# Optimization experiments

Hardware: AMD Instinct MI355X
Metric: run time of the kernel (lower is better)

Reference implementation:

```python
import jax, jax.numpy as jnp
import numpy as np

B, S, E = 8, 2048, 512
VOCAB, FVOCAB = 32000, 128
SCALE = float(np.power(E, 0.5))  # emb_size ** (0.5 * temper), temper=1


def setup_inputs() -> dict:
    key = jax.random.key(0)
    ks = jax.random.split(key, 7)
    key_seq = jax.random.randint(ks[0], (B, S), 0, VOCAB, dtype=jnp.int32)
    value_seq = jax.random.randint(ks[1], (B, S), 0, FVOCAB, dtype=jnp.int32)
    hidden = jax.random.normal(ks[2], (B, S, E), dtype=jnp.float32)
    mask_matrix = jax.random.uniform(ks[3], (B, S, S), dtype=jnp.float32)
    nan_matrix = jnp.zeros((1,), dtype=jnp.int32)  # unused by forward
    # learned params; padding_idx=0 -> zero row in embeddings
    key_emb = jax.random.normal(ks[4], (VOCAB, E), dtype=jnp.float32).at[0].set(0.0)
    value_emb = jax.random.normal(ks[5], (FVOCAB, E), dtype=jnp.float32).at[0].set(0.0)
    weight = jax.random.normal(ks[6], (E, E), dtype=jnp.float32) / np.sqrt(E)
    return {
        "key_seq": key_seq, "value_seq": value_seq, "hidden": hidden,
        "mask_matrix": mask_matrix, "nan_matrix": nan_matrix,
        "key_emb": key_emb, "value_emb": value_emb, "weight": weight,
    }


def reference(key_seq, value_seq, hidden, mask_matrix, nan_matrix,
              key_emb, value_emb, weight):
    k = key_emb[key_seq]          # [B,S,E]
    v = value_emb[value_seq]      # [B,S,E]
    q = jnp.einsum('bsd,de->bse', hidden, weight)   # hidden @ weight
    u = jnp.einsum('bse,bte->bst', q, k) / SCALE    # QK^T, [B,S,S]
    mask = jnp.clip(mask_matrix.astype(u.dtype), 0.0, 1.0)
    exp_u = jnp.exp(u)
    delta = exp_u * mask
    p = delta / (jnp.sum(delta, axis=2, keepdims=True) + 1e-10)
    o = jnp.einsum('bst,bte->bse', p, v)            # PV, [B,S,E]
    return o
```

## Files before the change

kernel.cpp:

```cpp
#include <hip/hip_runtime.h>
#include <stdint.h>

#define BB 8
#define SS 2048
#define EE 512
#define INV_SCALE 0.04419417382415922f

typedef __attribute__((ext_vector_type(8))) short bf8_t;
typedef __attribute__((ext_vector_type(4))) float f4_t;

__device__ __forceinline__ unsigned short f2bf(float f) {
    union { float f; uint32_t u; } x; x.f = f;
    uint32_t r = x.u + 0x7fffu + ((x.u >> 16) & 1u);
    return (unsigned short)(r >> 16);
}


__global__ void __launch_bounds__(256) gather_k_kernel(const int* __restrict__ idx,
                                                       const float* __restrict__ emb,
                                                       unsigned short* __restrict__ out) {
    int id = blockIdx.x * 256 + threadIdx.x;
    int chunk = id & 63;
    int row = id >> 6;
    int e0 = chunk * 8;
    int k = idx[row];
    const float* src = emb + (size_t)k * EE + e0;
    float4 a = *(const float4*)(src);
    float4 c = *(const float4*)(src + 4);
    union { unsigned short s[8]; int4 v; } u;
    u.s[0] = f2bf(a.x); u.s[1] = f2bf(a.y); u.s[2] = f2bf(a.z); u.s[3] = f2bf(a.w);
    u.s[4] = f2bf(c.x); u.s[5] = f2bf(c.y); u.s[6] = f2bf(c.z); u.s[7] = f2bf(c.w);
    *(int4*)(out + (size_t)row * EE + e0) = u.v;
}

__global__ void __launch_bounds__(256) cast_h_kernel(const float* __restrict__ in,
                                                     unsigned short* __restrict__ out) {
    int id = blockIdx.x * 256 + threadIdx.x;
    const float* src = in + (size_t)id * 8;
    float4 a = *(const float4*)(src);
    float4 c = *(const float4*)(src + 4);
    union { unsigned short s[8]; int4 v; } u;
    u.s[0] = f2bf(a.x); u.s[1] = f2bf(a.y); u.s[2] = f2bf(a.z); u.s[3] = f2bf(a.w);
    u.s[4] = f2bf(c.x); u.s[5] = f2bf(c.y); u.s[6] = f2bf(c.z); u.s[7] = f2bf(c.w);
    *(int4*)(out + (size_t)id * 8) = u.v;
}

__global__ void __launch_bounds__(256) gather_vt_kernel(const int* __restrict__ idx,
                                                        const float* __restrict__ emb,
                                                        unsigned short* __restrict__ vt) {
    int id = blockIdx.x * 256 + threadIdx.x;
    int t = id & (SS - 1);
    int rest = id >> 11;
    int e = rest & (EE - 1);
    int b = rest >> 9;
    int k = idx[b * SS + t];
    vt[id] = f2bf(emb[(size_t)k * EE + e]);
}

__global__ void __launch_bounds__(256) transpose_w_kernel(const float* __restrict__ w,
                                                          unsigned short* __restrict__ wt) {
    int id = blockIdx.x * 256 + threadIdx.x;
    int e = id & (EE - 1);
    int f = id >> 9;
    wt[id] = f2bf(w[(size_t)e * EE + f] * INV_SCALE);
}


__device__ __forceinline__ void stage_tile(const unsigned short* gbase, int ld, int k0,
                                           unsigned short* lds, int wave, int lane) {
    const int srcchunk = ((lane & 3) ^ ((lane >> 3) & 3)) * 8;
#pragma unroll
    for (int i = 0; i < 2; ++i) {
        int row = i * 64 + wave * 16 + (lane >> 2);
        const unsigned short* g = gbase + (size_t)row * ld + (k0 + srcchunk);
        unsigned short* l = lds + i * 2048 + wave * 512 + lane * 8;
        __builtin_amdgcn_global_load_lds((const __attribute__((address_space(1))) unsigned int*)g,
                                         (__attribute__((address_space(3))) unsigned int*)l,
                                         16, 0, 0);
    }
}

template <int KLEN>
__device__ __forceinline__ void mfma_loop(const unsigned short* Abase, int lda,
                                          const unsigned short* Bbase, int ldb,
                                          unsigned short* As, unsigned short* Bs,
                                          f4_t acc[4][4], int wave, int lane) {
    const int wm = wave >> 1, wn = wave & 1, quad = lane >> 4, l16 = lane & 15;
    const int qs = (quad ^ ((l16 >> 1) & 3)) * 8;
    constexpr int NT = KLEN / 32;

    stage_tile(Abase, lda, 0, As, wave, lane);
    stage_tile(Bbase, ldb, 0, Bs, wave, lane);
    __syncthreads();

    int cur = 0;
#pragma unroll 1
    for (int t = 0; t < NT; ++t) {
        if (t + 1 < NT) {
            stage_tile(Abase, lda, (t + 1) * 32, As + ((cur ^ 1) << 12), wave, lane);
            stage_tile(Bbase, ldb, (t + 1) * 32, Bs + ((cur ^ 1) << 12), wave, lane);
        }
        const unsigned short* a = As + (cur << 12);
        const unsigned short* b = Bs + (cur << 12);
        bf8_t af[4], bfr[4];
#pragma unroll
        for (int mi = 0; mi < 4; ++mi)
            af[mi] = *(const bf8_t*)(a + (wm * 64 + mi * 16 + l16) * 32 + qs);
#pragma unroll
        for (int ni = 0; ni < 4; ++ni)
            bfr[ni] = *(const bf8_t*)(b + (wn * 64 + ni * 16 + l16) * 32 + qs);
#pragma unroll
        for (int mi = 0; mi < 4; ++mi)
#pragma unroll
            for (int ni = 0; ni < 4; ++ni)
                acc[mi][ni] = __builtin_amdgcn_mfma_f32_16x16x32_bf16(af[mi], bfr[ni],
                                                                      acc[mi][ni], 0, 0, 0);
        __syncthreads();
        cur ^= 1;
    }
}

__global__ void __launch_bounds__(256) qgen_kernel(const unsigned short* __restrict__ H,
                                                   const unsigned short* __restrict__ Wt,
                                                   unsigned short* __restrict__ Q) {
    __shared__ unsigned short As[2 * 128 * 32];
    __shared__ unsigned short Bs[2 * 128 * 32];
    const int tid = threadIdx.x, wave = tid >> 6, lane = tid & 63;
    const int rowT = blockIdx.y;
    const int colT = blockIdx.x;
    f4_t acc[4][4];
    const f4_t z = {0.f, 0.f, 0.f, 0.f};
    for (int i = 0; i < 4; ++i) for (int j = 0; j < 4; ++j) acc[i][j] = z;
    mfma_loop<EE>(H + (size_t)rowT * 128 * EE, EE,
                  Wt + (size_t)colT * 128 * EE, EE, As, Bs, acc, wave, lane);
    const int wm = wave >> 1, wn = wave & 1, quad = lane >> 4, l16 = lane & 15;
#pragma unroll
    for (int mi = 0; mi < 4; ++mi)
#pragma unroll
        for (int r = 0; r < 4; ++r) {
            int row = rowT * 128 + wm * 64 + mi * 16 + quad * 4 + r;
#pragma unroll
            for (int ni = 0; ni < 4; ++ni) {
                int col = colT * 128 + wn * 64 + ni * 16 + l16;
                Q[(size_t)row * EE + col] = f2bf(acc[mi][ni][r]);
            }
        }
}

__global__ void __launch_bounds__(256) pv_kernel(const unsigned short* __restrict__ delta,
                                                 const unsigned short* __restrict__ Vt,
                                                 const float* __restrict__ lsum,
                                                 float* __restrict__ out) {
    __shared__ unsigned short As[2 * 128 * 32];
    __shared__ unsigned short Bs[2 * 128 * 32];
    const int tid = threadIdx.x, wave = tid >> 6, lane = tid & 63;
    const int b = blockIdx.z, qT = blockIdx.y, eT = blockIdx.x;
    f4_t acc[4][4];
    const f4_t z = {0.f, 0.f, 0.f, 0.f};
    for (int i = 0; i < 4; ++i) for (int j = 0; j < 4; ++j) acc[i][j] = z;
    mfma_loop<SS>(delta + ((size_t)b * SS + qT * 128) * SS, SS,
                  Vt + ((size_t)b * EE + eT * 128) * SS, SS, As, Bs, acc, wave, lane);
    const int wm = wave >> 1, wn = wave & 1, quad = lane >> 4, l16 = lane & 15;
#pragma unroll
    for (int mi = 0; mi < 4; ++mi)
#pragma unroll
        for (int r = 0; r < 4; ++r) {
            int row = qT * 128 + wm * 64 + mi * 16 + quad * 4 + r;
            float inv = 1.0f / (lsum[b * SS + row] + 1e-10f);
#pragma unroll
            for (int ni = 0; ni < 4; ++ni) {
                int col = eT * 128 + wn * 64 + ni * 16 + l16;
                out[((size_t)b * SS + row) * EE + col] = acc[mi][ni][r] * inv;
            }
        }
}


__device__ __forceinline__ void stage_half(const unsigned short* base, int t, int kh,
                                           unsigned short* half_, int tid) {
#pragma unroll
    for (int j = 0; j < 2; ++j) {
        int idx = j * 512 + tid;
        int r = idx >> 2, slot = idx & 3;
        int c4 = slot ^ ((r >> 1) & 3);
        const unsigned short* g = base + (size_t)r * EE + t * 64 + kh * 32 + c4 * 8;
        __builtin_amdgcn_global_load_lds((const __attribute__((address_space(1))) unsigned int*)g,
                                         (__attribute__((address_space(3))) unsigned int*)(half_ + idx * 8),
                                         16, 0, 0);
    }
}

template <int NH, int WAIT>
__device__ __forceinline__ void qk8_phase(const unsigned short* Ah, const unsigned short* Bh,
                                          bf8_t af[8], f4_t acc[8][4],
                                          const unsigned short* sbase, int st, int skh,
                                          unsigned short* sdst, bool sen,
                                          int wm, int wn, int l16, int aslot, int tid,
                                          bool lastsel) {
    if (NH == 0) {
#pragma unroll
        for (int mi = 0; mi < 8; ++mi)
            af[mi] = *(const bf8_t*)(Ah + (wm * 128 + mi * 16 + l16) * 32 + aslot);
    }
    bf8_t b0 = *(const bf8_t*)(Bh + (wn * 64 + NH * 32 + l16) * 32 + aslot);
    bf8_t b1 = *(const bf8_t*)(Bh + (wn * 64 + NH * 32 + 16 + l16) * 32 + aslot);
    if (sen) stage_half(sbase, st, skh, sdst, tid);
    if (WAIT >= 0) {
        if (lastsel) asm volatile("s_waitcnt vmcnt(0)" ::: "memory");
        else         asm volatile("s_waitcnt vmcnt(6)" ::: "memory");
    }
    __builtin_amdgcn_s_barrier();
    asm volatile("s_waitcnt lgkmcnt(0)" ::: "memory");
    __builtin_amdgcn_sched_barrier(0);
    __builtin_amdgcn_s_setprio(1);
#pragma unroll
    for (int mi = 0; mi < 8; ++mi) {
        acc[mi][NH * 2]     = __builtin_amdgcn_mfma_f32_16x16x32_bf16(af[mi], b0, acc[mi][NH * 2], 0, 0, 0);
        acc[mi][NH * 2 + 1] = __builtin_amdgcn_mfma_f32_16x16x32_bf16(af[mi], b1, acc[mi][NH * 2 + 1], 0, 0, 0);
    }
    __builtin_amdgcn_s_setprio(0);
    __builtin_amdgcn_s_barrier();
    __builtin_amdgcn_sched_barrier(0);
}

__global__ void __launch_bounds__(512, 2) qk8_kernel(const unsigned short* __restrict__ Q,
                                                     const unsigned short* __restrict__ K,
                                                     const float* __restrict__ mask,
                                                     unsigned short* __restrict__ delta,
                                                     float* __restrict__ lsum) {
    __shared__ unsigned short Ab[2][2][256 * 32];
    __shared__ unsigned short Bb[2][2][256 * 32];
    const int tid = threadIdx.x;
    const int wave = tid >> 6, lane = tid & 63;
    const int wm = wave >> 2, wn = wave & 3;
    const int quad = lane >> 4, l16 = lane & 15;
    const int aslot = (quad ^ ((l16 >> 1) & 3)) * 8;

    const int lin = blockIdx.x;
    const int b = lin & 7;
    const int rest = lin >> 3;
    const int tT = rest & 7, qT = rest >> 3;

    const unsigned short* Abase = Q + ((size_t)b * SS + qT * 256) * EE;
    const unsigned short* Bbase = K + ((size_t)b * SS + tT * 256) * EE;

    f4_t acc[8][4];
    const f4_t z = {0.f, 0.f, 0.f, 0.f};
#pragma unroll
    for (int i = 0; i < 8; ++i)
#pragma unroll
        for (int j = 0; j < 4; ++j) acc[i][j] = z;

    stage_half(Abase, 0, 0, &Ab[0][0][0], tid);
    stage_half(Bbase, 0, 0, &Bb[0][0][0], tid);
    stage_half(Abase, 0, 1, &Ab[0][1][0], tid);
    stage_half(Bbase, 0, 1, &Bb[0][1][0], tid);
    stage_half(Abase, 1, 0, &Ab[1][0][0], tid);
    stage_half(Bbase, 1, 0, &Bb[1][0][0], tid);
    stage_half(Abase, 1, 1, &Ab[1][1][0], tid);
    asm volatile("s_waitcnt vmcnt(6)" ::: "memory");
    __builtin_amdgcn_s_barrier();
    __builtin_amdgcn_sched_barrier(0);

    bf8_t af[8];

#pragma unroll 1
    for (int it = 0; it < 4; ++it) {
        const int t1 = 2 * it + 1, t2 = 2 * it + 2, t3 = 2 * it + 3;
        const bool last = (it == 3);
        qk8_phase<0, -1>(&Ab[0][0][0], &Bb[0][0][0], af, acc, Bbase, t1, 1, &Bb[1][1][0], true,  wm, wn, l16, aslot, tid, last);
        qk8_phase<1, -1>(&Ab[0][0][0], &Bb[0][0][0], af, acc, Abase, t2, 0, &Ab[0][0][0], !last, wm, wn, l16, aslot, tid, last);
        qk8_phase<0, -1>(&Ab[0][1][0], &Bb[0][1][0], af, acc, Bbase, t2, 0, &Bb[0][0][0], !last, wm, wn, l16, aslot, tid, last);
        qk8_phase<1,  6>(&Ab[0][1][0], &Bb[0][1][0], af, acc, Abase, t2, 1, &Ab[0][1][0], !last, wm, wn, l16, aslot, tid, last);
        qk8_phase<0, -1>(&Ab[1][0][0], &Bb[1][0][0], af, acc, Bbase, t2, 1, &Bb[0][1][0], !last, wm, wn, l16, aslot, tid, last);
        qk8_phase<1, -1>(&Ab[1][0][0], &Bb[1][0][0], af, acc, Abase, t3, 0, &Ab[1][0][0], !last, wm, wn, l16, aslot, tid, last);
        qk8_phase<0, -1>(&Ab[1][1][0], &Bb[1][1][0], af, acc, Bbase, t3, 0, &Bb[1][0][0], !last, wm, wn, l16, aslot, tid, last);
        qk8_phase<1,  6>(&Ab[1][1][0], &Bb[1][1][0], af, acc, Abase, t3, 1, &Ab[1][1][0], !last, wm, wn, l16, aslot, tid, last);
    }

#pragma unroll
    for (int mi = 0; mi < 8; ++mi) {
#pragma unroll
        for (int r = 0; r < 4; ++r) {
            int row = qT * 256 + wm * 128 + mi * 16 + quad * 4 + r;
            const float* mrow = mask + ((size_t)b * SS + row) * SS;
            unsigned short* drow = delta + ((size_t)b * SS + row) * SS;
            float psum = 0.f;
#pragma unroll
            for (int j = 0; j < 4; ++j) {
                int col = tT * 256 + wn * 64 + j * 16 + l16;
                float m = mrow[col];
                m = fminf(fmaxf(m, 0.f), 1.f);
                float e = __expf(acc[mi][j][r]) * m;
                drow[col] = f2bf(e);
                psum += e;
            }
#pragma unroll
            for (int off = 1; off < 16; off <<= 1)
                psum += __shfl_xor(psum, off, 16);
            if (l16 == 0) atomicAdd(&lsum[b * SS + row], psum);
        }
    }
}


extern "C" void kernel_launch(void* const* d_in, const int* in_sizes, int n_in,
                              void* d_out, int out_size, void* d_ws, size_t ws_size,
                              hipStream_t stream) {
    const int*   key_seq = (const int*)d_in[0];
    const int*   val_seq = (const int*)d_in[1];
    const float* hidden  = (const float*)d_in[2];
    const float* mask    = (const float*)d_in[3];
    const float* key_emb = (const float*)d_in[5];
    const float* val_emb = (const float*)d_in[6];
    const float* weight  = (const float*)d_in[7];
    float* out = (float*)d_out;

    char* ws = (char*)d_ws;
    const size_t SZ_BSE = (size_t)BB * SS * EE * sizeof(unsigned short);
    unsigned short* Q    = (unsigned short*)(ws);
    unsigned short* K    = (unsigned short*)(ws + SZ_BSE);
    unsigned short* Vt   = (unsigned short*)(ws + 2 * SZ_BSE);
    unsigned short* H    = (unsigned short*)(ws + 3 * SZ_BSE);
    unsigned short* Wt   = (unsigned short*)(ws + 4 * SZ_BSE);
    float*          lsum = (float*)(ws + 4 * SZ_BSE + 524288);
    unsigned short* delta= (unsigned short*)(ws + 4 * SZ_BSE + 524288 + 65536);

    hipMemsetAsync(lsum, 0, (size_t)BB * SS * sizeof(float), stream);

    gather_k_kernel<<<4096, 256, 0, stream>>>(key_seq, key_emb, K);
    cast_h_kernel<<<4096, 256, 0, stream>>>(hidden, H);
    gather_vt_kernel<<<32768, 256, 0, stream>>>(val_seq, val_emb, Vt);
    transpose_w_kernel<<<1024, 256, 0, stream>>>(weight, Wt);

    qgen_kernel<<<dim3(4, 128), 256, 0, stream>>>(H, Wt, Q);
    qk8_kernel<<<512, 512, 0, stream>>>(Q, K, mask, delta, lsum);
    pv_kernel<<<dim3(4, 16, 8), 256, 0, stream>>>(delta, Vt, lsum, out);
}
```

Measured before the change: 428.2 us.

## Replace PV GEMM with 256x128-tile, 8-wave pipelined kernel using direct-to-LDS loads

The old 128x128 PV kernel built on the generic mfma loop is replaced by a 512-thread kernel that computes 256x128 output tiles. It stages A/B halves into LDS with global_load_lds in a multi-buffered pipeline, using explicit vmcnt waits, barriers and setprio around the MFMA phases, and uses batch-interleaved block ordering. The V-transpose gather also writes 8 bf16 values per thread as one 16-byte store instead of one value per thread. This targets global-memory traffic and latency in the largest GEMM, at the cost of more registers and LDS per block and fragile hand-tuned wait counts.

```diff
diff --git a/kernel.cpp b/kernel.cpp
--- a/kernel.cpp
+++ b/kernel.cpp
@@ -49,12 +49,19 @@
                                                         const float* __restrict__ emb,
                                                         unsigned short* __restrict__ vt) {
     int id = blockIdx.x * 256 + threadIdx.x;
-    int t = id & (SS - 1);
-    int rest = id >> 11;
+    int t8 = id & 255;
+    int rest = id >> 8;
     int e = rest & (EE - 1);
     int b = rest >> 9;
-    int k = idx[b * SS + t];
-    vt[id] = f2bf(emb[(size_t)k * EE + e]);
+    int t0 = t8 * 8;
+    const int* ib = idx + b * SS + t0;
+    union { unsigned short s[8]; int4 v; } u;
+#pragma unroll
+    for (int j = 0; j < 8; ++j) {
+        int k = ib[j];
+        u.s[j] = f2bf(emb[(size_t)k * EE + e]);
+    }
+    *(int4*)(vt + ((size_t)b * EE + e) * SS + t0) = u.v;
 }
 
 __global__ void __launch_bounds__(256) transpose_w_kernel(const float* __restrict__ w,
@@ -147,34 +154,6 @@
         }
 }
 
-__global__ void __launch_bounds__(256) pv_kernel(const unsigned short* __restrict__ delta,
-                                                 const unsigned short* __restrict__ Vt,
-                                                 const float* __restrict__ lsum,
-                                                 float* __restrict__ out) {
-    __shared__ unsigned short As[2 * 128 * 32];
-    __shared__ unsigned short Bs[2 * 128 * 32];
-    const int tid = threadIdx.x, wave = tid >> 6, lane = tid & 63;
-    const int b = blockIdx.z, qT = blockIdx.y, eT = blockIdx.x;
-    f4_t acc[4][4];
-    const f4_t z = {0.f, 0.f, 0.f, 0.f};
-    for (int i = 0; i < 4; ++i) for (int j = 0; j < 4; ++j) acc[i][j] = z;
-    mfma_loop<SS>(delta + ((size_t)b * SS + qT * 128) * SS, SS,
-                  Vt + ((size_t)b * EE + eT * 128) * SS, SS, As, Bs, acc, wave, lane);
-    const int wm = wave >> 1, wn = wave & 1, quad = lane >> 4, l16 = lane & 15;
-#pragma unroll
-    for (int mi = 0; mi < 4; ++mi)
-#pragma unroll
-        for (int r = 0; r < 4; ++r) {
-            int row = qT * 128 + wm * 64 + mi * 16 + quad * 4 + r;
-            float inv = 1.0f / (lsum[b * SS + row] + 1e-10f);
-#pragma unroll
-            for (int ni = 0; ni < 4; ++ni) {
-                int col = eT * 128 + wn * 64 + ni * 16 + l16;
-                out[((size_t)b * SS + row) * EE + col] = acc[mi][ni][r] * inv;
-            }
-        }
-}
-
 
 __device__ __forceinline__ void stage_half(const unsigned short* base, int t, int kh,
                                            unsigned short* half_, int tid) {
@@ -304,6 +283,124 @@
 }
 
 
+__device__ __forceinline__ void stage_halfA(const unsigned short* base, int t, int kh,
+                                            unsigned short* half_, int tid) {
+#pragma unroll
+    for (int j = 0; j < 2; ++j) {
+        int idx = j * 512 + tid;
+        int r = idx >> 2, slot = idx & 3;
+        int c4 = slot ^ ((r >> 1) & 3);
+        const unsigned short* g = base + (size_t)r * SS + t * 64 + kh * 32 + c4 * 8;
+        __builtin_amdgcn_global_load_lds((const __attribute__((address_space(1))) unsigned int*)g,
+                                         (__attribute__((address_space(3))) unsigned int*)(half_ + idx * 8),
+                                         16, 0, 0);
+    }
+}
+
+__device__ __forceinline__ void stage_halfB(const unsigned short* base, int t, int kh,
+                                            unsigned short* half_, int tid) {
+    int r = tid >> 2, slot = tid & 3;
+    int c4 = slot ^ ((r >> 1) & 3);
+    const unsigned short* g = base + (size_t)r * SS + t * 64 + kh * 32 + c4 * 8;
+    __builtin_amdgcn_global_load_lds((const __attribute__((address_space(1))) unsigned int*)g,
+                                     (__attribute__((address_space(3))) unsigned int*)(half_ + tid * 8),
+                                     16, 0, 0);
+}
+
+template <int VM>
+__device__ __forceinline__ void pv8_phase(const unsigned short* Ah, const unsigned short* Bh,
+                                          f4_t acc[8][2],
+                                          const unsigned short* Abase, const unsigned short* Bbase,
+                                          int st, int skh, unsigned short* dA, unsigned short* dB,
+                                          bool sen,
+                                          int wm, int wn, int l16, int aslot, int tid) {
+    bf8_t af[8];
+#pragma unroll
+    for (int mi = 0; mi < 8; ++mi)
+        af[mi] = *(const bf8_t*)(Ah + (wm * 128 + mi * 16 + l16) * 32 + aslot);
+    bf8_t b0 = *(const bf8_t*)(Bh + (wn * 32 + l16) * 32 + aslot);
+    bf8_t b1 = *(const bf8_t*)(Bh + (wn * 32 + 16 + l16) * 32 + aslot);
+    if (sen) { stage_halfA(Abase, st, skh, dA, tid); stage_halfB(Bbase, st, skh, dB, tid); }
+    if (VM == 6)      asm volatile("s_waitcnt vmcnt(6)" ::: "memory");
+    else if (VM == 3) asm volatile("s_waitcnt vmcnt(3)" ::: "memory");
+    else              asm volatile("s_waitcnt vmcnt(0)" ::: "memory");
+    __builtin_amdgcn_s_barrier();
+    asm volatile("s_waitcnt lgkmcnt(0)" ::: "memory");
+    __builtin_amdgcn_sched_barrier(0);
+    __builtin_amdgcn_s_setprio(1);
+#pragma unroll
+    for (int mi = 0; mi < 8; ++mi) {
+        acc[mi][0] = __builtin_amdgcn_mfma_f32_16x16x32_bf16(af[mi], b0, acc[mi][0], 0, 0, 0);
+        acc[mi][1] = __builtin_amdgcn_mfma_f32_16x16x32_bf16(af[mi], b1, acc[mi][1], 0, 0, 0);
+    }
+    __builtin_amdgcn_s_setprio(0);
+    __builtin_amdgcn_s_barrier();
+    __builtin_amdgcn_sched_barrier(0);
+}
+
+__global__ void __launch_bounds__(512, 2) pv8_kernel(const unsigned short* __restrict__ delta,
+                                                     const unsigned short* __restrict__ Vt,
+                                                     const float* __restrict__ lsum,
+                                                     float* __restrict__ out) {
+    __shared__ unsigned short Ab[2][2][256 * 32];
+    __shared__ unsigned short Bb[2][2][128 * 32];
+    const int tid = threadIdx.x;
+    const int wave = tid >> 6, lane = tid & 63;
+    const int wm = wave >> 2, wn = wave & 3;
+    const int quad = lane >> 4, l16 = lane & 15;
+    const int aslot = (quad ^ ((l16 >> 1) & 3)) * 8;
+
+    const int lin = blockIdx.x;
+    const int b = lin & 7;
+    const int qT = (lin >> 3) & 7;
+    const int eT = lin >> 6;
+
+    const unsigned short* Abase = delta + ((size_t)b * SS + qT * 256) * SS;
+    const unsigned short* Bbase = Vt + ((size_t)b * EE + eT * 128) * SS;
+
+    f4_t acc[8][2];
+    const f4_t z = {0.f, 0.f, 0.f, 0.f};
+#pragma unroll
+    for (int i = 0; i < 8; ++i) { acc[i][0] = z; acc[i][1] = z; }
+
+    stage_halfA(Abase, 0, 0, &Ab[0][0][0], tid); stage_halfB(Bbase, 0, 0, &Bb[0][0][0], tid);
+    stage_halfA(Abase, 0, 1, &Ab[0][1][0], tid); stage_halfB(Bbase, 0, 1, &Bb[0][1][0], tid);
+    stage_halfA(Abase, 1, 0, &Ab[1][0][0], tid); stage_halfB(Bbase, 1, 0, &Bb[1][0][0], tid);
+    asm volatile("s_waitcnt vmcnt(6)" ::: "memory");
+    __builtin_amdgcn_s_barrier();
+    __builtin_amdgcn_sched_barrier(0);
+
+#pragma unroll 1
+    for (int it = 0; it < 16; ++it) {
+        const int t1 = 2 * it + 1, t2 = 2 * it + 2, t3 = 2 * it + 3;
+        if (it < 15) {
+            pv8_phase<6>(&Ab[0][0][0], &Bb[0][0][0], acc, Abase, Bbase, t1, 1, &Ab[1][1][0], &Bb[1][1][0], true, wm, wn, l16, aslot, tid);
+            pv8_phase<6>(&Ab[0][1][0], &Bb[0][1][0], acc, Abase, Bbase, t2, 0, &Ab[0][0][0], &Bb[0][0][0], true, wm, wn, l16, aslot, tid);
+            pv8_phase<6>(&Ab[1][0][0], &Bb[1][0][0], acc, Abase, Bbase, t2, 1, &Ab[0][1][0], &Bb[0][1][0], true, wm, wn, l16, aslot, tid);
+            pv8_phase<6>(&Ab[1][1][0], &Bb[1][1][0], acc, Abase, Bbase, t3, 0, &Ab[1][0][0], &Bb[1][0][0], true, wm, wn, l16, aslot, tid);
+        } else {
+            pv8_phase<6>(&Ab[0][0][0], &Bb[0][0][0], acc, Abase, Bbase, t1, 1, &Ab[1][1][0], &Bb[1][1][0], true, wm, wn, l16, aslot, tid);
+            pv8_phase<6>(&Ab[0][1][0], &Bb[0][1][0], acc, Abase, Bbase, 0, 0, (unsigned short*)0, (unsigned short*)0, false, wm, wn, l16, aslot, tid);
+            pv8_phase<3>(&Ab[1][0][0], &Bb[1][0][0], acc, Abase, Bbase, 0, 0, (unsigned short*)0, (unsigned short*)0, false, wm, wn, l16, aslot, tid);
+            pv8_phase<0>(&Ab[1][1][0], &Bb[1][1][0], acc, Abase, Bbase, 0, 0, (unsigned short*)0, (unsigned short*)0, false, wm, wn, l16, aslot, tid);
+        }
+    }
+
+#pragma unroll
+    for (int mi = 0; mi < 8; ++mi) {
+#pragma unroll
+        for (int r = 0; r < 4; ++r) {
+            const int row = qT * 256 + wm * 128 + mi * 16 + quad * 4 + r;
+            const float inv = 1.0f / (lsum[b * SS + row] + 1e-10f);
+            const size_t orow = ((size_t)b * SS + row) * EE;
+#pragma unroll
+            for (int nj = 0; nj < 2; ++nj)
+                out[orow + eT * 128 + wn * 32 + nj * 16 + l16] = acc[mi][nj][r] * inv;
+        }
+    }
+}
+
+
 extern "C" void kernel_launch(void* const* d_in, const int* in_sizes, int n_in,
                               void* d_out, int out_size, void* d_ws, size_t ws_size,
                               hipStream_t stream) {
@@ -330,10 +427,10 @@
 
     gather_k_kernel<<<4096, 256, 0, stream>>>(key_seq, key_emb, K);
     cast_h_kernel<<<4096, 256, 0, stream>>>(hidden, H);
-    gather_vt_kernel<<<32768, 256, 0, stream>>>(val_seq, val_emb, Vt);
+    gather_vt_kernel<<<4096, 256, 0, stream>>>(val_seq, val_emb, Vt);
     transpose_w_kernel<<<1024, 256, 0, stream>>>(weight, Wt);
 
     qgen_kernel<<<dim3(4, 128), 256, 0, stream>>>(H, Wt, Q);
     qk8_kernel<<<512, 512, 0, stream>>>(Q, K, mask, delta, lsum);
-    pv_kernel<<<dim3(4, 16, 8), 256, 0, stream>>>(delta, Vt, lsum, out);
-}
+    pv8_kernel<<<256, 512, 0, stream>>>(delta, Vt, lsum, out);
+}
```

After: 413.3 us. 1.04x faster.
